# Performance work log

Measured on AMD Instinct MI355X. Metric: run time of the kernel, lower is better.

## Reference

```python
import jax, jax.numpy as jnp
import numpy as np
import math

D_EMBED = 128
NUM_HEADS = 4
HEAD_DIM = D_EMBED // NUM_HEADS


def setup_inputs() -> dict:
    key = jax.random.key(0)
    k1, k2, k3 = jax.random.split(key, 3)
    x = jax.random.normal(k1, (4, D_EMBED, 64, 64), dtype=jnp.float32)
    # nn.Linear(d_embed, 3*d_embed): weight [3d, d], bias [3d]; store transposed for x @ W
    scale = 1.0 / math.sqrt(D_EMBED)
    W_qkv = jax.random.uniform(k2, (D_EMBED, 3 * D_EMBED), dtype=jnp.float32, minval=-scale, maxval=scale)
    b_qkv = jax.random.uniform(k3, (3 * D_EMBED,), dtype=jnp.float32, minval=-scale, maxval=scale)
    return {"x": x, "W_qkv": W_qkv, "b_qkv": b_qkv}


def reference(x, W_qkv, b_qkv):
    b, c, h, w = x.shape
    n = h * w
    hd = HEAD_DIM
    # (b, c, h, w) -> (b, n, c) tokens
    t = jnp.transpose(x.reshape(b, c, n), (0, 2, 1))
    qkv = t @ W_qkv + b_qkv  # (b, n, 3c)
    q, k, v = jnp.split(qkv, 3, axis=-1)
    # (b, n, c) -> (b, heads, n, hd)
    def to_heads(u):
        return jnp.transpose(u.reshape(b, n, NUM_HEADS, hd), (0, 2, 1, 3))
    q, k, v = to_heads(q), to_heads(k), to_heads(v)
    # full O(n^2) score matrix, as in the source
    scores = jnp.einsum('bhqd,bhkd->bhqk', q, k) / math.sqrt(hd)
    weights = jax.nn.softmax(scores, axis=-1)
    out = jnp.einsum('bhqk,bhkd->bhqd', weights, v)  # (b, heads, n, hd)
    # permute(0,2,1,3) -> (b, n, heads, hd), then raw reshape to input shape (as in source)
    out = jnp.transpose(out, (0, 2, 1, 3)).reshape(b, c, h, w)
    return out + x
```

## Files before the change

kernel.cpp:

```cpp
#include <hip/hip_runtime.h>
#include <hip/hip_bf16.h>

#define BB 4
#define CC 128
#define NN 4096
#define HH 4
#define HD 32
#define NTOK (BB*NN)

typedef float f32x4 __attribute__((ext_vector_type(4)));
typedef short bf16x8 __attribute__((ext_vector_type(8)));
typedef unsigned short u16;
typedef unsigned int u32;

__device__ __forceinline__ u16 f2bf(float f) {
    union { float f; u32 u; } v; v.f = f;
    u32 r = v.u + 0x7FFF + ((v.u >> 16) & 1);
    return (u16)(r >> 16);
}

__device__ __forceinline__ u32 cvtpk(float lo, float hi) {
    u32 r;
    asm("v_cvt_pk_bf16_f32 %0, %1, %2" : "=v"(r) : "v"(lo), "v"(hi));
    return r;
}

__global__ __launch_bounds__(256) void prep_kernel(const float* __restrict__ x,
                                                   const float* __restrict__ W,
                                                   u16* __restrict__ t_bf,
                                                   u16* __restrict__ Wt_bf) {
    __shared__ u16 tile[64][65];
    int blk = blockIdx.x;
    const float* src; u16* dst; int src_cols, dst_cols, r0, c0;
    if (blk < 512) {
        int b  = blk >> 7;
        int rem = blk & 127;
        int ct = rem >> 6;
        int nt = rem & 63;
        src = x + b * CC * NN;  src_cols = NN; r0 = ct * 64; c0 = nt * 64;
        dst = t_bf + b * NN * CC; dst_cols = CC;
    } else {
        int rem = blk - 512;
        int kt = rem / 6, nt = rem % 6;
        src = W; src_cols = 3 * CC; r0 = kt * 64; c0 = nt * 64;
        dst = Wt_bf; dst_cols = CC;
    }
    int t = threadIdx.x;
#pragma unroll
    for (int p = 0; p < 16; ++p) {
        int rl = p * 4 + (t >> 6);
        int cl = t & 63;
        tile[rl][cl] = f2bf(src[(r0 + rl) * src_cols + c0 + cl]);
    }
    __syncthreads();
#pragma unroll
    for (int p = 0; p < 16; ++p) {
        int cl = p * 4 + (t >> 6);
        int rl = t & 63;
        dst[(c0 + cl) * dst_cols + r0 + rl] = tile[rl][cl];
    }
}

__global__ __launch_bounds__(256, 2) void qkv_gemm(const u16* __restrict__ t_bf,
                                                   const u16* __restrict__ Wt_bf,
                                                   const float* __restrict__ bias,
                                                   u16* __restrict__ Qb,
                                                   u16* __restrict__ Kb,
                                                   u16* __restrict__ Vtb) {
    __shared__ u16 Al[128 * 128];
    __shared__ u16 Bl[128 * 128];
    int mt = blockIdx.x;
    int nt = blockIdx.y;
    int t = threadIdx.x;

    {
        const uint4* srcA = (const uint4*)(t_bf + mt * 128 * 128);
        const uint4* srcB = (const uint4*)(Wt_bf + nt * 128 * 128);
#pragma unroll
        for (int p = 0; p < 8; ++p) {
            int cid = p * 256 + t;
            int row = cid >> 4, c16 = cid & 15;
            int sw = (c16 ^ (row & 7)) * 8;
            *(uint4*)(Al + row * 128 + sw) = srcA[cid];
            *(uint4*)(Bl + row * 128 + sw) = srcB[cid];
        }
    }
    __syncthreads();

    int w = t >> 6, l = t & 63;
    int wq = (w >> 1) * 64, wn = (w & 1) * 64;
    int lr = l & 15, lg = l >> 4;

    f32x4 acc[4][4];
#pragma unroll
    for (int mi = 0; mi < 4; ++mi)
#pragma unroll
        for (int ni = 0; ni < 4; ++ni)
            acc[mi][ni] = f32x4{0.f, 0.f, 0.f, 0.f};

#pragma unroll
    for (int kk = 0; kk < 4; ++kk) {
        bf16x8 a[4], bb[4];
        int c = kk * 4 + lg;
#pragma unroll
        for (int mi = 0; mi < 4; ++mi) {
            int R = wq + mi * 16 + lr;
            a[mi] = *(const bf16x8*)(Al + R * 128 + ((c ^ (R & 7)) * 8));
        }
#pragma unroll
        for (int ni = 0; ni < 4; ++ni) {
            int R = wn + ni * 16 + lr;
            bb[ni] = *(const bf16x8*)(Bl + R * 128 + ((c ^ (R & 7)) * 8));
        }
#pragma unroll
        for (int mi = 0; mi < 4; ++mi)
#pragma unroll
            for (int ni = 0; ni < 4; ++ni)
                acc[mi][ni] = __builtin_amdgcn_mfma_f32_16x16x32_bf16(a[mi], bb[ni], acc[mi][ni], 0, 0, 0);
    }

    int b = mt >> 5;
    int tok0 = (mt & 31) * 128 + wq;
    if (nt == 2) {
#pragma unroll
        for (int mi = 0; mi < 4; ++mi)
#pragma unroll
            for (int ni = 0; ni < 4; ++ni) {
                int ch = wn + ni * 16 + lr;
                float bv = bias[256 + ch];
                int hh = ch >> 5, d = ch & 31;
                int tok = tok0 + mi * 16 + lg * 4;
                u16 tmp[4];
#pragma unroll
                for (int r = 0; r < 4; ++r) tmp[r] = f2bf(acc[mi][ni][r] + bv);
                *(uint2*)(Vtb + ((size_t)(b * HH + hh) * HD + d) * NN + tok) = *(uint2*)tmp;
            }
    } else {
        u16* outbuf = (nt == 0) ? Qb : Kb;
        float qscale = (nt == 0) ? 0.17677669529663687f : 1.0f;
#pragma unroll
        for (int mi = 0; mi < 4; ++mi)
#pragma unroll
            for (int ni = 0; ni < 4; ++ni) {
                int ch = wn + ni * 16 + lr;
                float bv = bias[nt * 128 + ch];
                int hh = ch >> 5, d = ch & 31;
#pragma unroll
                for (int r = 0; r < 4; ++r) {
                    int tok = tok0 + mi * 16 + lg * 4 + r;
                    float val = (acc[mi][ni][r] + bv) * qscale;
                    outbuf[((b * HH + hh) * NN + tok) * HD + d] = f2bf(val);
                }
            }
    }
}

__global__ __launch_bounds__(512, 4) void attn_kernel(const u16* __restrict__ Qb,
                                                      const u16* __restrict__ Kb,
                                                      const u16* __restrict__ Vtb,
                                                      const float* __restrict__ x,
                                                      float* __restrict__ out) {
    __shared__ __align__(16) u16 smem[8192];
    u16* KL = smem;
    u16* VL = smem + 2048;

    int tid = threadIdx.x;
    int w = tid >> 6, l = tid & 63;
    int lr = l & 15, lg = l >> 4;
    int bh = blockIdx.x;
    int qt = blockIdx.y;
    int b = bh >> 2, hh = bh & 3;
    int q0w = qt * 128 + w * 16;

    bf16x8 qa = *(const bf16x8*)(Qb + ((size_t)bh * NN + q0w + lr) * HD + lg * 8);

    int kRow = tid >> 3, kOff = (tid & 7) * 4;
    const u16* gK = Kb + ((size_t)bh * NN + kRow) * HD + kOff;
    u16* kDst = KL + kRow * 32 + kOff;
    int vD = tid >> 4, vC8 = tid & 15;
    const u16* gV = Vtb + ((size_t)bh * HD + vD) * NN + vC8 * 4;
    u16* vDst = VL + vD * 64 + ((vC8 ^ (vD & 15)) * 4);

    f32x4 acc0 = {0.f,0.f,0.f,0.f}, acc1 = {0.f,0.f,0.f,0.f};
    float m = -1e30f, ll = 0.f;
    const float L2E = 1.44269504f;
    union PB { u32 w4[4]; bf16x8 v; };

    for (int kt = 0; kt < 64; ++kt) {
        uint2 kreg = *(const uint2*)(gK + (size_t)kt * 64 * HD);
        uint2 vreg = *(const uint2*)(gV + kt * 64);
        __syncthreads();
        *(uint2*)kDst = kreg;
        *(uint2*)vDst = vreg;
        __syncthreads();

        bf16x8 ka0 = *(const bf16x8*)(KL + (lr     ) * 32 + lg * 8);
        bf16x8 ka1 = *(const bf16x8*)(KL + (16 + lr) * 32 + lg * 8);
        bf16x8 ka2 = *(const bf16x8*)(KL + (32 + lr) * 32 + lg * 8);
        bf16x8 ka3 = *(const bf16x8*)(KL + (48 + lr) * 32 + lg * 8);
        f32x4 z = {0.f,0.f,0.f,0.f};
        f32x4 s0 = __builtin_amdgcn_mfma_f32_16x16x32_bf16(ka0, qa, z, 0, 0, 0);
        f32x4 s1 = __builtin_amdgcn_mfma_f32_16x16x32_bf16(ka1, qa, z, 0, 0, 0);
        f32x4 s2 = __builtin_amdgcn_mfma_f32_16x16x32_bf16(ka2, qa, z, 0, 0, 0);
        f32x4 s3 = __builtin_amdgcn_mfma_f32_16x16x32_bf16(ka3, qa, z, 0, 0, 0);

        float t0 = fmaxf(fmaxf(s0[0], s0[1]), fmaxf(s0[2], s0[3]));
        float t1 = fmaxf(fmaxf(s1[0], s1[1]), fmaxf(s1[2], s1[3]));
        float t2 = fmaxf(fmaxf(s2[0], s2[1]), fmaxf(s2[2], s2[3]));
        float t3 = fmaxf(fmaxf(s3[0], s3[1]), fmaxf(s3[2], s3[3]));
        float pmax = fmaxf(fmaxf(t0, t1), fmaxf(t2, t3));
        pmax = fmaxf(pmax, __shfl_xor(pmax, 16));
        pmax = fmaxf(pmax, __shfl_xor(pmax, 32));
        float mnew = fmaxf(m, pmax);
        float alpha = __builtin_amdgcn_exp2f((m - mnew) * L2E);
        m = mnew;
        float mm = m * L2E;
#define EXPX(vv) vv = __builtin_amdgcn_exp2f(__builtin_fmaf(vv, L2E, -mm))
        EXPX(s0[0]); EXPX(s0[1]); EXPX(s0[2]); EXPX(s0[3]);
        EXPX(s1[0]); EXPX(s1[1]); EXPX(s1[2]); EXPX(s1[3]);
        EXPX(s2[0]); EXPX(s2[1]); EXPX(s2[2]); EXPX(s2[3]);
        EXPX(s3[0]); EXPX(s3[1]); EXPX(s3[2]); EXPX(s3[3]);
#undef EXPX
        float psum = ((s0[0] + s0[1]) + (s0[2] + s0[3]))
                   + ((s1[0] + s1[1]) + (s1[2] + s1[3]))
                   + ((s2[0] + s2[1]) + (s2[2] + s2[3]))
                   + ((s3[0] + s3[1]) + (s3[2] + s3[3]));
        psum += __shfl_xor(psum, 16);
        psum += __shfl_xor(psum, 32);
        ll = ll * alpha + psum;
        acc0 *= alpha; acc1 *= alpha;

        PB p0, p1;
        p0.w4[0] = cvtpk(s0[0], s0[1]); p0.w4[1] = cvtpk(s0[2], s0[3]);
        p0.w4[2] = cvtpk(s1[0], s1[1]); p0.w4[3] = cvtpk(s1[2], s1[3]);
        p1.w4[0] = cvtpk(s2[0], s2[1]); p1.w4[1] = cvtpk(s2[2], s2[3]);
        p1.w4[2] = cvtpk(s3[0], s3[1]); p1.w4[3] = cvtpk(s3[2], s3[3]);

#pragma unroll
        for (int dt = 0; dt < 2; ++dt) {
            int dd = dt * 16 + lr;
#pragma unroll
            for (int ks = 0; ks < 2; ++ks) {
                uint2 a0 = *(const uint2*)(VL + dd * 64 + ((ks * 8 + lg)     ^ lr) * 4);
                uint2 a1 = *(const uint2*)(VL + dd * 64 + ((ks * 8 + 4 + lg) ^ lr) * 4);
                PB va;
                va.w4[0] = a0.x; va.w4[1] = a0.y; va.w4[2] = a1.x; va.w4[3] = a1.y;
                f32x4& ac = dt ? acc1 : acc0;
                ac = __builtin_amdgcn_mfma_f32_16x16x32_bf16(va.v, (ks ? p1 : p0).v, ac, 0, 0, 0);
            }
        }
    }
    __syncthreads();

    float inv = 1.0f / ll;
    acc0 *= inv; acc1 *= inv;

    float* OW = (float*)smem + w * 512;
    *(f32x4*)(OW + lr * 32 + ((lg    ) ^ (lr & 7)) * 4) = acc0;
    *(f32x4*)(OW + lr * 32 + ((4 + lg) ^ (lr & 7)) * 4) = acc1;
    int q = l & 15, part = l >> 4;
    f32x4 r0 = *(const f32x4*)(OW + q * 32 + ((2 * part    ) ^ (q & 7)) * 4);
    f32x4 r1 = *(const f32x4*)(OW + q * 32 + ((2 * part + 1) ^ (q & 7)) * 4);

    size_t gbase = ((size_t)b * NN + q0w + q) * CC + hh * 32 + part * 8;
    f32x4 x0 = *(const f32x4*)(x + gbase);
    f32x4 x1 = *(const f32x4*)(x + gbase + 4);
    *(f32x4*)(out + gbase)     = r0 + x0;
    *(f32x4*)(out + gbase + 4) = r1 + x1;
}

extern "C" void kernel_launch(void* const* d_in, const int* in_sizes, int n_in,
                              void* d_out, int out_size, void* d_ws, size_t ws_size,
                              hipStream_t stream) {
    const float* x   = (const float*)d_in[0];
    const float* W   = (const float*)d_in[1];
    const float* bia = (const float*)d_in[2];
    float* out = (float*)d_out;

    char* ws = (char*)d_ws;
    size_t off = 0;
    u16* t_bf  = (u16*)(ws + off); off += (size_t)NTOK * CC * 2;
    u16* Wt_bf = (u16*)(ws + off); off += (size_t)384 * 128 * 2;
    u16* Qb    = (u16*)(ws + off); off += (size_t)BB * HH * NN * HD * 2;
    u16* Kb    = (u16*)(ws + off); off += (size_t)BB * HH * NN * HD * 2;
    u16* Vtb   = (u16*)(ws + off); off += (size_t)BB * HH * NN * HD * 2;

    hipLaunchKernelGGL(prep_kernel, dim3(524), dim3(256), 0, stream, x, W, t_bf, Wt_bf);
    hipLaunchKernelGGL(qkv_gemm, dim3(128, 3), dim3(256), 0, stream, t_bf, Wt_bf, bia, Qb, Kb, Vtb);
    hipLaunchKernelGGL(attn_kernel, dim3(16, 32), dim3(512), 0, stream, Qb, Kb, Vtb, x, out);
}
```

Measured before the change: 149.1 us.

## Process two query subtiles per wave in attention to reuse K/V fragments

```diff
diff --git a/kernel.cpp b/kernel.cpp
--- a/kernel.cpp
+++ b/kernel.cpp
@@ -155,14 +155,14 @@
     }
 }
 
-__global__ __launch_bounds__(512, 4) void attn_kernel(const u16* __restrict__ Qb,
+__global__ __launch_bounds__(256, 2) void attn_kernel(const u16* __restrict__ Qb,
                                                       const u16* __restrict__ Kb,
                                                       const u16* __restrict__ Vtb,
                                                       const float* __restrict__ x,
                                                       float* __restrict__ out) {
-    __shared__ __align__(16) u16 smem[8192];
+    __shared__ __align__(16) u16 smem[7168];
     u16* KL = smem;
-    u16* VL = smem + 2048;
+    u16* VL = smem + 2560;
 
     int tid = threadIdx.x;
     int w = tid >> 6, l = tid & 63;
@@ -170,103 +170,155 @@
     int bh = blockIdx.x;
     int qt = blockIdx.y;
     int b = bh >> 2, hh = bh & 3;
-    int q0w = qt * 128 + w * 16;
-
-    bf16x8 qa = *(const bf16x8*)(Qb + ((size_t)bh * NN + q0w + lr) * HD + lg * 8);
-
-    int kRow = tid >> 3, kOff = (tid & 7) * 4;
+    int q0w = qt * 128 + w * 32;
+
+    bf16x8 qa0 = *(const bf16x8*)(Qb + ((size_t)bh * NN + q0w + lr     ) * HD + lg * 8);
+    bf16x8 qa1 = *(const bf16x8*)(Qb + ((size_t)bh * NN + q0w + 16 + lr) * HD + lg * 8);
+
+    int kRow = tid >> 2, kOff = (tid & 3) * 8;
     const u16* gK = Kb + ((size_t)bh * NN + kRow) * HD + kOff;
-    u16* kDst = KL + kRow * 32 + kOff;
-    int vD = tid >> 4, vC8 = tid & 15;
-    const u16* gV = Vtb + ((size_t)bh * HD + vD) * NN + vC8 * 4;
-    u16* vDst = VL + vD * 64 + ((vC8 ^ (vD & 15)) * 4);
-
-    f32x4 acc0 = {0.f,0.f,0.f,0.f}, acc1 = {0.f,0.f,0.f,0.f};
-    float m = -1e30f, ll = 0.f;
+    u16* kDst = KL + kRow * 40 + kOff;
+    int vD = tid >> 3, vC16 = tid & 7;
+    const u16* gV = Vtb + ((size_t)bh * HD + vD) * NN + vC16 * 8;
+    u16* vDstA = VL + vD * 64 + (((2 * vC16)     ^ (vD & 15)) * 4);
+    u16* vDstB = VL + vD * 64 + (((2 * vC16 + 1) ^ (vD & 15)) * 4);
+
+    f32x4 a00 = {0.f,0.f,0.f,0.f}, a01 = {0.f,0.f,0.f,0.f};
+    f32x4 a10 = {0.f,0.f,0.f,0.f}, a11 = {0.f,0.f,0.f,0.f};
+    float m0 = -1e30f, ll0 = 0.f, m1 = -1e30f, ll1 = 0.f;
     const float L2E = 1.44269504f;
     union PB { u32 w4[4]; bf16x8 v; };
 
     for (int kt = 0; kt < 64; ++kt) {
-        uint2 kreg = *(const uint2*)(gK + (size_t)kt * 64 * HD);
-        uint2 vreg = *(const uint2*)(gV + kt * 64);
+        uint4 kreg = *(const uint4*)(gK + (size_t)kt * 64 * HD);
+        uint4 vreg = *(const uint4*)(gV + kt * 64);
         __syncthreads();
-        *(uint2*)kDst = kreg;
-        *(uint2*)vDst = vreg;
+        *(uint4*)kDst = kreg;
+        *(uint2*)vDstA = make_uint2(vreg.x, vreg.y);
+        *(uint2*)vDstB = make_uint2(vreg.z, vreg.w);
         __syncthreads();
 
-        bf16x8 ka0 = *(const bf16x8*)(KL + (lr     ) * 32 + lg * 8);
-        bf16x8 ka1 = *(const bf16x8*)(KL + (16 + lr) * 32 + lg * 8);
-        bf16x8 ka2 = *(const bf16x8*)(KL + (32 + lr) * 32 + lg * 8);
-        bf16x8 ka3 = *(const bf16x8*)(KL + (48 + lr) * 32 + lg * 8);
+        bf16x8 ka0 = *(const bf16x8*)(KL + (lr     ) * 40 + lg * 8);
+        bf16x8 ka1 = *(const bf16x8*)(KL + (16 + lr) * 40 + lg * 8);
+        bf16x8 ka2 = *(const bf16x8*)(KL + (32 + lr) * 40 + lg * 8);
+        bf16x8 ka3 = *(const bf16x8*)(KL + (48 + lr) * 40 + lg * 8);
         f32x4 z = {0.f,0.f,0.f,0.f};
-        f32x4 s0 = __builtin_amdgcn_mfma_f32_16x16x32_bf16(ka0, qa, z, 0, 0, 0);
-        f32x4 s1 = __builtin_amdgcn_mfma_f32_16x16x32_bf16(ka1, qa, z, 0, 0, 0);
-        f32x4 s2 = __builtin_amdgcn_mfma_f32_16x16x32_bf16(ka2, qa, z, 0, 0, 0);
-        f32x4 s3 = __builtin_amdgcn_mfma_f32_16x16x32_bf16(ka3, qa, z, 0, 0, 0);
-
-        float t0 = fmaxf(fmaxf(s0[0], s0[1]), fmaxf(s0[2], s0[3]));
-        float t1 = fmaxf(fmaxf(s1[0], s1[1]), fmaxf(s1[2], s1[3]));
-        float t2 = fmaxf(fmaxf(s2[0], s2[1]), fmaxf(s2[2], s2[3]));
-        float t3 = fmaxf(fmaxf(s3[0], s3[1]), fmaxf(s3[2], s3[3]));
-        float pmax = fmaxf(fmaxf(t0, t1), fmaxf(t2, t3));
-        pmax = fmaxf(pmax, __shfl_xor(pmax, 16));
-        pmax = fmaxf(pmax, __shfl_xor(pmax, 32));
-        float mnew = fmaxf(m, pmax);
-        float alpha = __builtin_amdgcn_exp2f((m - mnew) * L2E);
-        m = mnew;
-        float mm = m * L2E;
-#define EXPX(vv) vv = __builtin_amdgcn_exp2f(__builtin_fmaf(vv, L2E, -mm))
-        EXPX(s0[0]); EXPX(s0[1]); EXPX(s0[2]); EXPX(s0[3]);
-        EXPX(s1[0]); EXPX(s1[1]); EXPX(s1[2]); EXPX(s1[3]);
-        EXPX(s2[0]); EXPX(s2[1]); EXPX(s2[2]); EXPX(s2[3]);
-        EXPX(s3[0]); EXPX(s3[1]); EXPX(s3[2]); EXPX(s3[3]);
+
+        f32x4 s0 = __builtin_amdgcn_mfma_f32_16x16x32_bf16(ka0, qa0, z, 0, 0, 0);
+        f32x4 s1 = __builtin_amdgcn_mfma_f32_16x16x32_bf16(ka1, qa0, z, 0, 0, 0);
+        f32x4 s2 = __builtin_amdgcn_mfma_f32_16x16x32_bf16(ka2, qa0, z, 0, 0, 0);
+        f32x4 s3 = __builtin_amdgcn_mfma_f32_16x16x32_bf16(ka3, qa0, z, 0, 0, 0);
+        f32x4 u0 = __builtin_amdgcn_mfma_f32_16x16x32_bf16(ka0, qa1, z, 0, 0, 0);
+        f32x4 u1 = __builtin_amdgcn_mfma_f32_16x16x32_bf16(ka1, qa1, z, 0, 0, 0);
+        f32x4 u2 = __builtin_amdgcn_mfma_f32_16x16x32_bf16(ka2, qa1, z, 0, 0, 0);
+        f32x4 u3 = __builtin_amdgcn_mfma_f32_16x16x32_bf16(ka3, qa1, z, 0, 0, 0);
+
+#define EXPX(vv, mmv) vv = __builtin_amdgcn_exp2f(__builtin_fmaf(vv, L2E, -mmv))
+        PB p0, p1;
+        {
+            float t0 = fmaxf(fmaxf(s0[0], s0[1]), fmaxf(s0[2], s0[3]));
+            float t1 = fmaxf(fmaxf(s1[0], s1[1]), fmaxf(s1[2], s1[3]));
+            float t2 = fmaxf(fmaxf(s2[0], s2[1]), fmaxf(s2[2], s2[3]));
+            float t3 = fmaxf(fmaxf(s3[0], s3[1]), fmaxf(s3[2], s3[3]));
+            float pmax = fmaxf(fmaxf(t0, t1), fmaxf(t2, t3));
+            pmax = fmaxf(pmax, __shfl_xor(pmax, 16));
+            pmax = fmaxf(pmax, __shfl_xor(pmax, 32));
+            float mnew = fmaxf(m0, pmax);
+            float alpha = __builtin_amdgcn_exp2f((m0 - mnew) * L2E);
+            m0 = mnew;
+            float mm = m0 * L2E;
+            EXPX(s0[0], mm); EXPX(s0[1], mm); EXPX(s0[2], mm); EXPX(s0[3], mm);
+            EXPX(s1[0], mm); EXPX(s1[1], mm); EXPX(s1[2], mm); EXPX(s1[3], mm);
+            EXPX(s2[0], mm); EXPX(s2[1], mm); EXPX(s2[2], mm); EXPX(s2[3], mm);
+            EXPX(s3[0], mm); EXPX(s3[1], mm); EXPX(s3[2], mm); EXPX(s3[3], mm);
+            float psum = ((s0[0] + s0[1]) + (s0[2] + s0[3]))
+                       + ((s1[0] + s1[1]) + (s1[2] + s1[3]))
+                       + ((s2[0] + s2[1]) + (s2[2] + s2[3]))
+                       + ((s3[0] + s3[1]) + (s3[2] + s3[3]));
+            ll0 = ll0 * alpha + psum;
+            a00 *= alpha; a01 *= alpha;
+            p0.w4[0] = cvtpk(s0[0], s0[1]); p0.w4[1] = cvtpk(s0[2], s0[3]);
+            p0.w4[2] = cvtpk(s1[0], s1[1]); p0.w4[3] = cvtpk(s1[2], s1[3]);
+            p1.w4[0] = cvtpk(s2[0], s2[1]); p1.w4[1] = cvtpk(s2[2], s2[3]);
+            p1.w4[2] = cvtpk(s3[0], s3[1]); p1.w4[3] = cvtpk(s3[2], s3[3]);
+        }
+        PB p2, p3;
+        {
+            float t0 = fmaxf(fmaxf(u0[0], u0[1]), fmaxf(u0[2], u0[3]));
+            float t1 = fmaxf(fmaxf(u1[0], u1[1]), fmaxf(u1[2], u1[3]));
+            float t2 = fmaxf(fmaxf(u2[0], u2[1]), fmaxf(u2[2], u2[3]));
+            float t3 = fmaxf(fmaxf(u3[0], u3[1]), fmaxf(u3[2], u3[3]));
+            float pmax = fmaxf(fmaxf(t0, t1), fmaxf(t2, t3));
+            pmax = fmaxf(pmax, __shfl_xor(pmax, 16));
+            pmax = fmaxf(pmax, __shfl_xor(pmax, 32));
+            float mnew = fmaxf(m1, pmax);
+            float alpha = __builtin_amdgcn_exp2f((m1 - mnew) * L2E);
+            m1 = mnew;
+            float mm = m1 * L2E;
+            EXPX(u0[0], mm); EXPX(u0[1], mm); EXPX(u0[2], mm); EXPX(u0[3], mm);
+            EXPX(u1[0], mm); EXPX(u1[1], mm); EXPX(u1[2], mm); EXPX(u1[3], mm);
+            EXPX(u2[0], mm); EXPX(u2[1], mm); EXPX(u2[2], mm); EXPX(u2[3], mm);
+            EXPX(u3[0], mm); EXPX(u3[1], mm); EXPX(u3[2], mm); EXPX(u3[3], mm);
+            float psum = ((u0[0] + u0[1]) + (u0[2] + u0[3]))
+                       + ((u1[0] + u1[1]) + (u1[2] + u1[3]))
+                       + ((u2[0] + u2[1]) + (u2[2] + u2[3]))
+                       + ((u3[0] + u3[1]) + (u3[2] + u3[3]));
+            ll1 = ll1 * alpha + psum;
+            a10 *= alpha; a11 *= alpha;
+            p2.w4[0] = cvtpk(u0[0], u0[1]); p2.w4[1] = cvtpk(u0[2], u0[3]);
+            p2.w4[2] = cvtpk(u1[0], u1[1]); p2.w4[3] = cvtpk(u1[2], u1[3]);
+            p3.w4[0] = cvtpk(u2[0], u2[1]); p3.w4[1] = cvtpk(u2[2], u2[3]);
+            p3.w4[2] = cvtpk(u3[0], u3[1]); p3.w4[3] = cvtpk(u3[2], u3[3]);
+        }
 #undef EXPX
-        float psum = ((s0[0] + s0[1]) + (s0[2] + s0[3]))
-                   + ((s1[0] + s1[1]) + (s1[2] + s1[3]))
-                   + ((s2[0] + s2[1]) + (s2[2] + s2[3]))
-                   + ((s3[0] + s3[1]) + (s3[2] + s3[3]));
-        psum += __shfl_xor(psum, 16);
-        psum += __shfl_xor(psum, 32);
-        ll = ll * alpha + psum;
-        acc0 *= alpha; acc1 *= alpha;
-
-        PB p0, p1;
-        p0.w4[0] = cvtpk(s0[0], s0[1]); p0.w4[1] = cvtpk(s0[2], s0[3]);
-        p0.w4[2] = cvtpk(s1[0], s1[1]); p0.w4[3] = cvtpk(s1[2], s1[3]);
-        p1.w4[0] = cvtpk(s2[0], s2[1]); p1.w4[1] = cvtpk(s2[2], s2[3]);
-        p1.w4[2] = cvtpk(s3[0], s3[1]); p1.w4[3] = cvtpk(s3[2], s3[3]);
 
 #pragma unroll
         for (int dt = 0; dt < 2; ++dt) {
             int dd = dt * 16 + lr;
 #pragma unroll
             for (int ks = 0; ks < 2; ++ks) {
-                uint2 a0 = *(const uint2*)(VL + dd * 64 + ((ks * 8 + lg)     ^ lr) * 4);
-                uint2 a1 = *(const uint2*)(VL + dd * 64 + ((ks * 8 + 4 + lg) ^ lr) * 4);
+                uint2 va0 = *(const uint2*)(VL + dd * 64 + ((ks * 8 + lg)     ^ lr) * 4);
+                uint2 va1 = *(const uint2*)(VL + dd * 64 + ((ks * 8 + 4 + lg) ^ lr) * 4);
                 PB va;
-                va.w4[0] = a0.x; va.w4[1] = a0.y; va.w4[2] = a1.x; va.w4[3] = a1.y;
-                f32x4& ac = dt ? acc1 : acc0;
-                ac = __builtin_amdgcn_mfma_f32_16x16x32_bf16(va.v, (ks ? p1 : p0).v, ac, 0, 0, 0);
+                va.w4[0] = va0.x; va.w4[1] = va0.y; va.w4[2] = va1.x; va.w4[3] = va1.y;
+                f32x4& c0 = dt ? a01 : a00;
+                f32x4& c1 = dt ? a11 : a10;
+                c0 = __builtin_amdgcn_mfma_f32_16x16x32_bf16(va.v, (ks ? p1 : p0).v, c0, 0, 0, 0);
+                c1 = __builtin_amdgcn_mfma_f32_16x16x32_bf16(va.v, (ks ? p3 : p2).v, c1, 0, 0, 0);
             }
         }
     }
     __syncthreads();
 
-    float inv = 1.0f / ll;
-    acc0 *= inv; acc1 *= inv;
+    ll0 += __shfl_xor(ll0, 16); ll0 += __shfl_xor(ll0, 32);
+    ll1 += __shfl_xor(ll1, 16); ll1 += __shfl_xor(ll1, 32);
+    float inv0 = 1.0f / ll0, inv1 = 1.0f / ll1;
+    a00 *= inv0; a01 *= inv0; a10 *= inv1; a11 *= inv1;
 
     float* OW = (float*)smem + w * 512;
-    *(f32x4*)(OW + lr * 32 + ((lg    ) ^ (lr & 7)) * 4) = acc0;
-    *(f32x4*)(OW + lr * 32 + ((4 + lg) ^ (lr & 7)) * 4) = acc1;
     int q = l & 15, part = l >> 4;
-    f32x4 r0 = *(const f32x4*)(OW + q * 32 + ((2 * part    ) ^ (q & 7)) * 4);
-    f32x4 r1 = *(const f32x4*)(OW + q * 32 + ((2 * part + 1) ^ (q & 7)) * 4);
-
-    size_t gbase = ((size_t)b * NN + q0w + q) * CC + hh * 32 + part * 8;
-    f32x4 x0 = *(const f32x4*)(x + gbase);
-    f32x4 x1 = *(const f32x4*)(x + gbase + 4);
-    *(f32x4*)(out + gbase)     = r0 + x0;
-    *(f32x4*)(out + gbase + 4) = r1 + x1;
+    {
+        *(f32x4*)(OW + lr * 32 + ((lg    ) ^ (lr & 7)) * 4) = a00;
+        *(f32x4*)(OW + lr * 32 + ((4 + lg) ^ (lr & 7)) * 4) = a01;
+        f32x4 r0 = *(const f32x4*)(OW + q * 32 + ((2 * part    ) ^ (q & 7)) * 4);
+        f32x4 r1 = *(const f32x4*)(OW + q * 32 + ((2 * part + 1) ^ (q & 7)) * 4);
+        size_t gbase = ((size_t)b * NN + q0w + q) * CC + hh * 32 + part * 8;
+        f32x4 x0 = *(const f32x4*)(x + gbase);
+        f32x4 x1 = *(const f32x4*)(x + gbase + 4);
+        *(f32x4*)(out + gbase)     = r0 + x0;
+        *(f32x4*)(out + gbase + 4) = r1 + x1;
+    }
+    {
+        *(f32x4*)(OW + lr * 32 + ((lg    ) ^ (lr & 7)) * 4) = a10;
+        *(f32x4*)(OW + lr * 32 + ((4 + lg) ^ (lr & 7)) * 4) = a11;
+        f32x4 r0 = *(const f32x4*)(OW + q * 32 + ((2 * part    ) ^ (q & 7)) * 4);
+        f32x4 r1 = *(const f32x4*)(OW + q * 32 + ((2 * part + 1) ^ (q & 7)) * 4);
+        size_t gbase = ((size_t)b * NN + q0w + 16 + q) * CC + hh * 32 + part * 8;
+        f32x4 x0 = *(const f32x4*)(x + gbase);
+        f32x4 x1 = *(const f32x4*)(x + gbase + 4);
+        *(f32x4*)(out + gbase)     = r0 + x0;
+        *(f32x4*)(out + gbase + 4) = r1 + x1;
+    }
 }
 
 extern "C" void kernel_launch(void* const* d_in, const int* in_sizes, int n_in,
@@ -287,5 +339,5 @@
 
     hipLaunchKernelGGL(prep_kernel, dim3(524), dim3(256), 0, stream, x, W, t_bf, Wt_bf);
     hipLaunchKernelGGL(qkv_gemm, dim3(128, 3), dim3(256), 0, stream, t_bf, Wt_bf, bia, Qb, Kb, Vtb);
-    hipLaunchKernelGGL(attn_kernel, dim3(16, 32), dim3(512), 0, stream, Qb, Kb, Vtb, x, out);
-}
+    hipLaunchKernelGGL(attn_kernel, dim3(16, 32), dim3(256), 0, stream, Qb, Kb, Vtb, x, out);
+}
```

Measured after the change: 148.0 us. Within noise of the previous version (-0.8%).
